# Kernel optimization log

Hardware: AMD Instinct MI355X
Metric: run time of the kernel (lower is better)

The kernel has to match this reference:

```python
import jax, jax.numpy as jnp
import numpy as np

K = 8        # number of nearest neighbors (idw default)
POWER = 2    # inverse-distance power (idw default)
EPS = 1e-8


def setup_inputs() -> dict:
    key = jax.random.key(0)
    kq, kr, kf = jax.random.split(key, 3)
    N, M = 32768, 16384
    # scale coords so points are spread out like real LiDAR scenes
    query_points = jax.random.normal(kq, (N, 3), dtype=jnp.float32) * 10.0
    ref_points = jax.random.normal(kr, (M, 3), dtype=jnp.float32) * 10.0
    ref_flow = jax.random.normal(kf, (M, 3), dtype=jnp.float32)
    return {"query_points": query_points, "ref_points": ref_points, "ref_flow": ref_flow}


def reference(query_points, ref_points, ref_flow):
    # cdist: Euclidean distance [N, M] via (q-r)^2 = |q|^2 + |r|^2 - 2 q.r
    q2 = jnp.sum(query_points * query_points, axis=-1, keepdims=True)      # [N,1]
    r2 = jnp.sum(ref_points * ref_points, axis=-1)                          # [M]
    d2 = q2 + r2 - 2.0 * (query_points @ ref_points.T)                      # [N,M]
    dist = jnp.sqrt(jnp.maximum(d2, 0.0))
    # k smallest distances == top_k of negated distances
    neg_knn, knn_idx = jax.lax.top_k(-dist, K)                               # [N,K]
    knn_dist = -neg_knn
    # inverse-distance weights: 1 / (d^power + eps), normalized over k
    weights = 1.0 / (knn_dist ** POWER + EPS)
    weights = weights / jnp.sum(weights, axis=1, keepdims=True)
    knn_flow = ref_flow[knn_idx]                                             # [N,K,3]
    return jnp.sum(weights[..., None] * knn_flow, axis=1)                    # [N,3]
```

## Files before the change

kernel.cpp:

```cpp
#include <hip/hip_runtime.h>

#define KNN    8
#define BLOCK  256
#define TILE   2048
#define GD     32
#define NC     (GD*GD*GD)
#define EPSW   1e-8f
#define BIGF   3.4e38f

__device__ __forceinline__ void insert8(float d2, int j, float bd[KNN], int bi[KNN]) {
    if (d2 < bd[0]) {
        bd[0] = d2; bi[0] = j;
#pragma unroll
        for (int t = 0; t < KNN - 1; t++) {
            if (bd[t] < bd[t + 1]) {
                float td = bd[t]; bd[t] = bd[t + 1]; bd[t + 1] = td;
                int   ti = bi[t]; bi[t] = bi[t + 1]; bi[t + 1] = ti;
            }
        }
    }
}

__device__ __forceinline__ void ced(float& a, int& ai, float& b, int& bi) {
    if (a < b) { float t = a; a = b; b = t; int ti = ai; ai = bi; bi = ti; }
}
__device__ __forceinline__ void sort8_desc(float d[KNN], int ix[KNN]) {
    ced(d[0],ix[0],d[4],ix[4]); ced(d[1],ix[1],d[5],ix[5]);
    ced(d[2],ix[2],d[6],ix[6]); ced(d[3],ix[3],d[7],ix[7]);
    ced(d[0],ix[0],d[2],ix[2]); ced(d[1],ix[1],d[3],ix[3]);
    ced(d[4],ix[4],d[6],ix[6]); ced(d[5],ix[5],d[7],ix[7]);
    ced(d[0],ix[0],d[1],ix[1]); ced(d[2],ix[2],d[3],ix[3]);
    ced(d[4],ix[4],d[5],ix[5]); ced(d[6],ix[6],d[7],ix[7]);
}
__device__ __forceinline__ void merge_lists(float bd[KNN], int bi[KNN], int mask, bool sort_after) {
    float pd[KNN]; int pi[KNN];
#pragma unroll
    for (int j = 0; j < KNN; j++) { pd[j] = __shfl_xor(bd[j], mask); pi[j] = __shfl_xor(bi[j], mask); }
#pragma unroll
    for (int j = 0; j < KNN; j++) {
        if (pd[KNN - 1 - j] < bd[j]) { bd[j] = pd[KNN - 1 - j]; bi[j] = pi[KNN - 1 - j]; }
    }
    if (sort_after) sort8_desc(bd, bi);
}
__device__ __forceinline__ float merged_thr4(const float bd[KNN]) {
    float c[KNN], p[KNN];
#pragma unroll
    for (int j = 0; j < KNN; j++) c[j] = bd[j];
#pragma unroll
    for (int j = 0; j < KNN; j++) p[j] = __shfl_xor(c[j], 1);
#pragma unroll
    for (int j = 0; j < KNN; j++) c[j] = fminf(c[j], p[KNN - 1 - j]);
    {
        float mx, mn;
        mx = fmaxf(c[0],c[4]); mn = fminf(c[0],c[4]); c[0]=mx; c[4]=mn;
        mx = fmaxf(c[1],c[5]); mn = fminf(c[1],c[5]); c[1]=mx; c[5]=mn;
        mx = fmaxf(c[2],c[6]); mn = fminf(c[2],c[6]); c[2]=mx; c[6]=mn;
        mx = fmaxf(c[3],c[7]); mn = fminf(c[3],c[7]); c[3]=mx; c[7]=mn;
        mx = fmaxf(c[0],c[2]); mn = fminf(c[0],c[2]); c[0]=mx; c[2]=mn;
        mx = fmaxf(c[1],c[3]); mn = fminf(c[1],c[3]); c[1]=mx; c[3]=mn;
        mx = fmaxf(c[4],c[6]); mn = fminf(c[4],c[6]); c[4]=mx; c[6]=mn;
        mx = fmaxf(c[5],c[7]); mn = fminf(c[5],c[7]); c[5]=mx; c[7]=mn;
        mx = fmaxf(c[0],c[1]); mn = fminf(c[0],c[1]); c[0]=mx; c[1]=mn;
        mx = fmaxf(c[2],c[3]); mn = fminf(c[2],c[3]); c[2]=mx; c[3]=mn;
        mx = fmaxf(c[4],c[5]); mn = fminf(c[4],c[5]); c[4]=mx; c[5]=mn;
        mx = fmaxf(c[6],c[7]); mn = fminf(c[6],c[7]); c[6]=mx; c[7]=mn;
    }
#pragma unroll
    for (int j = 0; j < KNN; j++) p[j] = __shfl_xor(c[j], 2);
#pragma unroll
    for (int j = 0; j < KNN; j++) c[j] = fminf(c[j], p[KNN - 1 - j]);
    float m = c[0];
#pragma unroll
    for (int j = 1; j < KNN; j++) m = fmaxf(m, c[j]);
    return m;
}

__device__ __forceinline__ unsigned fenc(float f) {
    unsigned u = __float_as_uint(f);
    return (u & 0x80000000u) ? ~u : (u | 0x80000000u);
}
__device__ __forceinline__ float fdec(unsigned e) {
    unsigned u = (e & 0x80000000u) ? (e ^ 0x80000000u) : ~e;
    return __uint_as_float(u);
}

__device__ __forceinline__ void load_bb(const unsigned* __restrict__ bbw,
                                        float mn[3], float inv[3], float& hmin) {
    hmin = BIGF;
#pragma unroll
    for (int a = 0; a < 3; a++) {
        float lo = fdec(bbw[a]), hi = -fdec(bbw[3 + a]);
        float w = fmaxf(hi - lo, 1e-9f);
        mn[a] = lo;
        inv[a] = (float)GD / w;
        hmin = fminf(hmin, w / (float)GD);
    }
}

__device__ __forceinline__ int cell_clamp(int c) {
    return c < 0 ? 0 : (c > GD - 1 ? GD - 1 : c);
}


__global__ __launch_bounds__(256) void bbox_zero(const float* __restrict__ r, int M,
                                                 unsigned* __restrict__ bbw,
                                                 int* __restrict__ zbase, int zcount) {
    int idx = blockIdx.x * 256 + threadIdx.x;
    for (int j = idx; j < zcount; j += gridDim.x * 256) zbase[j] = 0;
    float mn0 = BIGF, mn1 = BIGF, mn2 = BIGF;
    float mx0 = -BIGF, mx1 = -BIGF, mx2 = -BIGF;
    for (int j = idx; j < M; j += gridDim.x * 256) {
        float x = r[3 * j], y = r[3 * j + 1], z = r[3 * j + 2];
        mn0 = fminf(mn0, x); mx0 = fmaxf(mx0, x);
        mn1 = fminf(mn1, y); mx1 = fmaxf(mx1, y);
        mn2 = fminf(mn2, z); mx2 = fmaxf(mx2, z);
    }
#pragma unroll
    for (int o = 32; o > 0; o >>= 1) {
        mn0 = fminf(mn0, __shfl_xor(mn0, o));
        mn1 = fminf(mn1, __shfl_xor(mn1, o));
        mn2 = fminf(mn2, __shfl_xor(mn2, o));
        mx0 = fmaxf(mx0, __shfl_xor(mx0, o));
        mx1 = fmaxf(mx1, __shfl_xor(mx1, o));
        mx2 = fmaxf(mx2, __shfl_xor(mx2, o));
    }
    if ((threadIdx.x & 63) == 0) {
        atomicMin(bbw + 0, fenc(mn0)); atomicMin(bbw + 1, fenc(mn1)); atomicMin(bbw + 2, fenc(mn2));
        atomicMin(bbw + 3, fenc(-mx0)); atomicMin(bbw + 4, fenc(-mx1)); atomicMin(bbw + 5, fenc(-mx2));
    }
}

__global__ __launch_bounds__(256) void hist2(const float* __restrict__ r,
                                             const float* __restrict__ q,
                                             int M, int N, const unsigned* __restrict__ bbw,
                                             int* __restrict__ rcid, int* __restrict__ qcid,
                                             int* __restrict__ rcnt, int* __restrict__ qcnt) {
    float mn[3], inv[3], hmin;
    load_bb(bbw, mn, inv, hmin);
    int i = blockIdx.x * 256 + threadIdx.x;
    if (i < M) {
        int cx = cell_clamp((int)((r[3 * i]     - mn[0]) * inv[0]));
        int cy = cell_clamp((int)((r[3 * i + 1] - mn[1]) * inv[1]));
        int cz = cell_clamp((int)((r[3 * i + 2] - mn[2]) * inv[2]));
        int cid = (cz * GD + cy) * GD + cx;
        rcid[i] = cid;
        atomicAdd(rcnt + cid, 1);
    } else if (i < M + N) {
        int j = i - M;
        int cx = cell_clamp((int)((q[3 * j]     - mn[0]) * inv[0]));
        int cy = cell_clamp((int)((q[3 * j + 1] - mn[1]) * inv[1]));
        int cz = cell_clamp((int)((q[3 * j + 2] - mn[2]) * inv[2]));
        int cid = (cz * GD + cy) * GD + cx;
        qcid[j] = cid;
        atomicAdd(qcnt + cid, 1);
    }
}

__global__ __launch_bounds__(1024) void scan2(int* __restrict__ rcnt, int* __restrict__ rstart,
                                              int* __restrict__ qcnt, int* __restrict__ qstart) {
    int* cnt = (blockIdx.x == 0) ? rcnt : qcnt;
    int* st  = (blockIdx.x == 0) ? rstart : qstart;
    __shared__ int part[1024];
    int t = threadIdx.x;
    int base = t * 32;
    int s = 0;
#pragma unroll
    for (int k = 0; k < 32; k++) s += cnt[base + k];
    part[t] = s;
    __syncthreads();
    for (int off = 1; off < 1024; off <<= 1) {
        int v = (t >= off) ? part[t - off] : 0;
        __syncthreads();
        part[t] += v;
        __syncthreads();
    }
    int run = part[t] - s;
#pragma unroll
    for (int k = 0; k < 32; k++) {
        int c = cnt[base + k];
        st[base + k] = run;
        cnt[base + k] = run;
        run += c;
    }
    if (t == 1023) st[NC] = run;
}

__global__ __launch_bounds__(256) void scatter2(const float* __restrict__ r,
                                                const float* __restrict__ q, int M, int N,
                                                const int* __restrict__ rcid,
                                                const int* __restrict__ qcid,
                                                int* __restrict__ rcur, int* __restrict__ qcur,
                                                float4* __restrict__ rps, int* __restrict__ sidx,
                                                float4* __restrict__ qps, int* __restrict__ qorder) {
    int i = blockIdx.x * 256 + threadIdx.x;
    if (i < M) {
        int pos = atomicAdd(rcur + rcid[i], 1);
        float x = r[3 * i], y = r[3 * i + 1], z = r[3 * i + 2];
        rps[pos] = make_float4(x, y, z, x * x + y * y + z * z);
        sidx[pos] = i;
    } else if (i < M + N) {
        int j = i - M;
        int pos = atomicAdd(qcur + qcid[j], 1);
        float x = q[3 * j], y = q[3 * j + 1], z = q[3 * j + 2];
        qps[pos] = make_float4(x, y, z, x * x + y * y + z * z);
        qorder[pos] = j;
    }
}

__device__ __forceinline__ void scan_shell(
    int R, int cx, int cy, int cz, int sub,
    const float4* __restrict__ rps, const int* __restrict__ rstart,
    float qx, float qy, float qz, float q2,
    float bd[KNN], int bi[KNN], float& thr) {
    for (int dz = -R; dz <= R; ++dz) {
        int z = cz + dz;
        if ((unsigned)z >= GD) continue;
        for (int dy = -R; dy <= R; ++dy) {
            int y = cy + dy;
            if ((unsigned)y >= GD) continue;
            int rowb = (z * GD + y) * GD;
            if (dz == -R || dz == R || dy == -R || dy == R) {
                int x0 = max(cx - R, 0), x1 = min(cx + R, GD - 1);
                int s = rstart[rowb + x0], e = rstart[rowb + x1 + 1];
                for (int ii = s + sub; ii < e; ii += 4) {
                    float4 p = rps[ii];
                    float d2 = (q2 + p.w) - 2.0f * (qx * p.x + qy * p.y + qz * p.z);
                    if (d2 < thr) { insert8(d2, ii, bd, bi); thr = bd[0]; }
                }
            } else {
                int xl = cx - R, xr = cx + R;
                if (xl >= 0) {
                    int s = rstart[rowb + xl], e = rstart[rowb + xl + 1];
                    for (int ii = s + sub; ii < e; ii += 4) {
                        float4 p = rps[ii];
                        float d2 = (q2 + p.w) - 2.0f * (qx * p.x + qy * p.y + qz * p.z);
                        if (d2 < thr) { insert8(d2, ii, bd, bi); thr = bd[0]; }
                    }
                }
                if (xr < GD) {
                    int s = rstart[rowb + xr], e = rstart[rowb + xr + 1];
                    for (int ii = s + sub; ii < e; ii += 4) {
                        float4 p = rps[ii];
                        float d2 = (q2 + p.w) - 2.0f * (qx * p.x + qy * p.y + qz * p.z);
                        if (d2 < thr) { insert8(d2, ii, bd, bi); thr = bd[0]; }
                    }
                }
            }
        }
    }
}

__global__ __launch_bounds__(256) void knn_pass1(
    const float4* __restrict__ rps, const int* __restrict__ rstart,
    const float4* __restrict__ qps, const int* __restrict__ qorder,
    const int* __restrict__ sidx, const float* __restrict__ f,
    const unsigned* __restrict__ bbw, float* __restrict__ out,
    int* __restrict__ pend, int* __restrict__ pcnt, int N) {
    int t = blockIdx.x * 256 + threadIdx.x;
    int g = t >> 2;
    int sub = t & 3;
    if (g >= N) return;
    int qi = qorder[g];
    float4 qp = qps[g];
    float qx = qp.x, qy = qp.y, qz = qp.z, q2 = qp.w;
    float mn[3], inv[3], hmin;
    load_bb(bbw, mn, inv, hmin);
    int cx = cell_clamp((int)((qx - mn[0]) * inv[0]));
    int cy = cell_clamp((int)((qy - mn[1]) * inv[1]));
    int cz = cell_clamp((int)((qz - mn[2]) * inv[2]));

    float bd[KNN]; int bi[KNN];
#pragma unroll
    for (int k = 0; k < KNN; k++) { bd[k] = BIGF; bi[k] = 0; }
    float thr = BIGF;

    int rs[9], re[9];
#pragma unroll
    for (int dz = -1; dz <= 1; dz++) {
#pragma unroll
        for (int dy = -1; dy <= 1; dy++) {
            int k = (dz + 1) * 3 + (dy + 1);
            int z = cz + dz, y = cy + dy;
            if ((unsigned)z >= GD || (unsigned)y >= GD) { rs[k] = 0; re[k] = 0; }
            else {
                int rowb = (z * GD + y) * GD;
                int x0 = max(cx - 1, 0), x1 = min(cx + 1, GD - 1);
                rs[k] = rstart[rowb + x0]; re[k] = rstart[rowb + x1 + 1];
            }
        }
    }
#pragma unroll
    for (int k = 0; k < 9; k++) {
        for (int ii = rs[k] + sub; ii < re[k]; ii += 4) {
            float4 p = rps[ii];
            float d2 = (q2 + p.w) - 2.0f * (qx * p.x + qy * p.y + qz * p.z);
            if (d2 < thr) { insert8(d2, ii, bd, bi); thr = bd[0]; }
        }
    }
    float mthr = merged_thr4(bd);
    thr = fminf(thr, mthr);
    bool done = (mthr <= hmin * hmin);

    if (!done) {
        scan_shell(2, cx, cy, cz, sub, rps, rstart, qx, qy, qz, q2, bd, bi, thr);
        mthr = merged_thr4(bd);
        done = (mthr <= 4.0f * hmin * hmin);
    }

    if (!done) {
        if (sub == 0) { int pos = atomicAdd(pcnt, 1); pend[pos] = qi; }
        return;
    }

    merge_lists(bd, bi, 1, true);
    merge_lists(bd, bi, 2, false);
    if (sub == 0) {
        float wsum = 0.f, ox = 0.f, oy = 0.f, oz = 0.f;
#pragma unroll
        for (int k = 0; k < KNN; k++) {
            float w = 1.0f / (fmaxf(bd[k], 0.0f) + EPSW);
            int j = sidx[bi[k]];
            wsum += w;
            ox += w * f[3 * j];
            oy += w * f[3 * j + 1];
            oz += w * f[3 * j + 2];
        }
        float invw = 1.0f / wsum;
        out[3 * qi]     = ox * invw;
        out[3 * qi + 1] = oy * invw;
        out[3 * qi + 2] = oz * invw;
    }
}

__global__ __launch_bounds__(256) void knn_pass2(
    const float4* __restrict__ rps, const int* __restrict__ pend,
    const int* __restrict__ pcnt, const float* __restrict__ q,
    const int* __restrict__ sidx, const float* __restrict__ f,
    float* __restrict__ out, int M) {
    __shared__ float sd[4][KNN];
    __shared__ int   si[4][KNN];
    int tid = threadIdx.x;
    int lane = tid & 63, wv = tid >> 6;
    int cnt = *pcnt;
    for (int w = blockIdx.x; w < cnt; w += gridDim.x) {
        int qi = pend[w];
        float qx = q[3 * qi], qy = q[3 * qi + 1], qz = q[3 * qi + 2];
        float q2 = qx * qx + qy * qy + qz * qz;
        float bd[KNN]; int bi[KNN];
#pragma unroll
        for (int k = 0; k < KNN; k++) { bd[k] = BIGF; bi[k] = 0; }
        float thr = BIGF;
        int i = tid;
        for (; i + 1792 < M; i += 2048) {
            float4 p0 = rps[i];
            float4 p1 = rps[i + 256];
            float4 p2 = rps[i + 512];
            float4 p3 = rps[i + 768];
            float4 p4 = rps[i + 1024];
            float4 p5 = rps[i + 1280];
            float4 p6 = rps[i + 1536];
            float4 p7 = rps[i + 1792];
            float d0 = (q2 + p0.w) - 2.0f * (qx * p0.x + qy * p0.y + qz * p0.z);
            float d1 = (q2 + p1.w) - 2.0f * (qx * p1.x + qy * p1.y + qz * p1.z);
            float d2 = (q2 + p2.w) - 2.0f * (qx * p2.x + qy * p2.y + qz * p2.z);
            float d3 = (q2 + p3.w) - 2.0f * (qx * p3.x + qy * p3.y + qz * p3.z);
            float d4 = (q2 + p4.w) - 2.0f * (qx * p4.x + qy * p4.y + qz * p4.z);
            float d5 = (q2 + p5.w) - 2.0f * (qx * p5.x + qy * p5.y + qz * p5.z);
            float d6 = (q2 + p6.w) - 2.0f * (qx * p6.x + qy * p6.y + qz * p6.z);
            float d7 = (q2 + p7.w) - 2.0f * (qx * p7.x + qy * p7.y + qz * p7.z);
            if (d0 < thr) { insert8(d0, i,        bd, bi); thr = bd[0]; }
            if (d1 < thr) { insert8(d1, i + 256,  bd, bi); thr = bd[0]; }
            if (d2 < thr) { insert8(d2, i + 512,  bd, bi); thr = bd[0]; }
            if (d3 < thr) { insert8(d3, i + 768,  bd, bi); thr = bd[0]; }
            if (d4 < thr) { insert8(d4, i + 1024, bd, bi); thr = bd[0]; }
            if (d5 < thr) { insert8(d5, i + 1280, bd, bi); thr = bd[0]; }
            if (d6 < thr) { insert8(d6, i + 1536, bd, bi); thr = bd[0]; }
            if (d7 < thr) { insert8(d7, i + 1792, bd, bi); thr = bd[0]; }
        }
        for (; i < M; i += 256) {
            float4 p = rps[i];
            float d2 = (q2 + p.w) - 2.0f * (qx * p.x + qy * p.y + qz * p.z);
            if (d2 < thr) { insert8(d2, i, bd, bi); thr = bd[0]; }
        }
        merge_lists(bd, bi, 1, true);
        merge_lists(bd, bi, 2, true);
        merge_lists(bd, bi, 4, true);
        merge_lists(bd, bi, 8, true);
        merge_lists(bd, bi, 16, true);
        merge_lists(bd, bi, 32, true);
        if (lane == 0) {
#pragma unroll
            for (int k = 0; k < KNN; k++) { sd[wv][k] = bd[k]; si[wv][k] = bi[k]; }
        }
        __syncthreads();
        if (tid == 0) {
            for (int v = 1; v < 4; v++) {
#pragma unroll
                for (int k = 0; k < KNN; k++) insert8(sd[v][k], si[v][k], bd, bi);
            }
            float wsum = 0.f, ox = 0.f, oy = 0.f, oz = 0.f;
#pragma unroll
            for (int k = 0; k < KNN; k++) {
                float wgt = 1.0f / (fmaxf(bd[k], 0.0f) + EPSW);
                int j = sidx[bi[k]];
                wsum += wgt;
                ox += wgt * f[3 * j];
                oy += wgt * f[3 * j + 1];
                oz += wgt * f[3 * j + 2];
            }
            float invw = 1.0f / wsum;
            out[3 * qi]     = ox * invw;
            out[3 * qi + 1] = oy * invw;
            out[3 * qi + 2] = oz * invw;
        }
        __syncthreads();
    }
}

__global__ __launch_bounds__(BLOCK) void knn_fused(
    const float* __restrict__ q, const float* __restrict__ r,
    const float* __restrict__ f, float* __restrict__ out, int N, int M) {
    __shared__ float4 lds[TILE];
    int qi = blockIdx.x * BLOCK + threadIdx.x;
    float qx = 0.f, qy = 0.f, qz = 0.f, q2 = 0.f;
    if (qi < N) {
        qx = q[3 * qi]; qy = q[3 * qi + 1]; qz = q[3 * qi + 2];
        q2 = qx * qx + qy * qy + qz * qz;
    }
    float bd[KNN]; int bi[KNN];
#pragma unroll
    for (int k = 0; k < KNN; k++) { bd[k] = BIGF; bi[k] = 0; }
    for (int tb = 0; tb < M; tb += TILE) {
        int cnt = min(TILE, M - tb);
        for (int i = threadIdx.x; i < cnt; i += BLOCK) {
            int j = tb + i;
            float rx = r[3 * j], ry = r[3 * j + 1], rz = r[3 * j + 2];
            lds[i] = make_float4(rx, ry, rz, rx * rx + ry * ry + rz * rz);
        }
        __syncthreads();
        for (int i = 0; i < cnt; i++) {
            float4 p = lds[i];
            float d2 = (q2 + p.w) - 2.0f * (qx * p.x + qy * p.y + qz * p.z);
            insert8(d2, tb + i, bd, bi);
        }
        __syncthreads();
    }
    if (qi < N) {
        float wsum = 0.f, ox = 0.f, oy = 0.f, oz = 0.f;
#pragma unroll
        for (int k = 0; k < KNN; k++) {
            float w = 1.0f / (fmaxf(bd[k], 0.0f) + EPSW);
            int j = bi[k];
            ox += w * f[3 * j];
            oy += w * f[3 * j + 1];
            oz += w * f[3 * j + 2];
        }
        float inv = 1.0f / wsum;
        out[3 * qi]     = ox * inv;
        out[3 * qi + 1] = oy * inv;
        out[3 * qi + 2] = oz * inv;
    }
}

extern "C" void kernel_launch(void* const* d_in, const int* in_sizes, int n_in,
                              void* d_out, int out_size, void* d_ws, size_t ws_size,
                              hipStream_t stream) {
    const float* q = (const float*)d_in[0];
    const float* r = (const float*)d_in[1];
    const float* f = (const float*)d_in[2];
    float* out = (float*)d_out;
    int N = in_sizes[0] / 3;
    int M = in_sizes[1] / 3;

    size_t off = 0;
    auto take = [&](size_t b) { size_t o = off; off += (b + 255) & ~(size_t)255; return o; };
    size_t o_rps  = take((size_t)M * 16);
    size_t o_qps  = take((size_t)N * 16);
    size_t o_sidx = take((size_t)M * 4);
    size_t o_rcid = take((size_t)M * 4);
    size_t o_qcid = take((size_t)N * 4);
    size_t o_qord = take((size_t)N * 4);
    size_t o_rst  = take((size_t)(NC + 1) * 4);
    size_t o_qst  = take((size_t)(NC + 1) * 4);
    size_t o_rcur = take((size_t)NC * 4);
    size_t o_qcur = take((size_t)NC * 4);
    size_t o_pcnt = take(4);
    size_t o_pend = take((size_t)N * 4);
    size_t o_bb   = take(64);

    int grid_x = (N + BLOCK - 1) / BLOCK;
    if (off <= ws_size) {
        char* w = (char*)d_ws;
        float4* rps   = (float4*)(w + o_rps);
        float4* qps   = (float4*)(w + o_qps);
        int* sidx     = (int*)(w + o_sidx);
        int* rcid     = (int*)(w + o_rcid);
        int* qcid     = (int*)(w + o_qcid);
        int* qorder   = (int*)(w + o_qord);
        int* rstart   = (int*)(w + o_rst);
        int* qstart   = (int*)(w + o_qst);
        int* rcur     = (int*)(w + o_rcur);
        int* qcur     = (int*)(w + o_qcur);
        int* pcnt     = (int*)(w + o_pcnt);
        int* pend     = (int*)(w + o_pend);
        unsigned* bbw = (unsigned*)(w + o_bb);

        hipMemsetAsync(w + o_bb, 0xFF, 24, stream);

        int zcount = (int)((o_pcnt + 4 - o_rcur) / 4);
        int g_all = (M + N + 255) / 256;
        bbox_zero<<<64, 256, 0, stream>>>(r, M, bbw, rcur, zcount);
        hist2<<<g_all, 256, 0, stream>>>(r, q, M, N, bbw, rcid, qcid, rcur, qcur);
        scan2<<<2, 1024, 0, stream>>>(rcur, rstart, qcur, qstart);
        scatter2<<<g_all, 256, 0, stream>>>(r, q, M, N, rcid, qcid, rcur, qcur,
                                            rps, sidx, qps, qorder);
        int g_p1 = (int)(((size_t)N * 4 + 255) / 256);
        knn_pass1<<<g_p1, 256, 0, stream>>>(rps, rstart, qps, qorder, sidx, f, bbw, out,
                                            pend, pcnt, N);
        knn_pass2<<<4096, 256, 0, stream>>>(rps, pend, pcnt, q, sidx, f, out, M);
    } else {
        knn_fused<<<grid_x, BLOCK, 0, stream>>>(q, r, f, out, N, M);
    }
}
```

Measured before the change: 196.8 us.

## Fuse grid-build kernels into one cooperative kernel with grid syncs

Replaces the memset plus bbox, histogram, scan and scatter launches with a single cooperative kernel of 256 blocks that separates the phases with grid-wide syncs. The aim is to remove per-launch overhead and inter-kernel gaps in the preprocessing stage. In exchange, the scan runs with 256 threads per block, each handling more cells serially. Grid syncs add their own cost, and the cooperative launch needs all 256 blocks to be co-resident on the device.

```diff
diff --git a/kernel.cpp b/kernel.cpp
--- a/kernel.cpp
+++ b/kernel.cpp
@@ -1,4 +1,7 @@
 #include <hip/hip_runtime.h>
+#include <hip/hip_cooperative_groups.h>
+
+namespace cg = cooperative_groups;
 
 #define KNN    8
 #define BLOCK  256
@@ -101,109 +104,114 @@
     return c < 0 ? 0 : (c > GD - 1 ? GD - 1 : c);
 }
 
-
-__global__ __launch_bounds__(256) void bbox_zero(const float* __restrict__ r, int M,
-                                                 unsigned* __restrict__ bbw,
-                                                 int* __restrict__ zbase, int zcount) {
+__global__ __launch_bounds__(256) void grid_build(
+    const float* __restrict__ r, const float* __restrict__ q, int M, int N,
+    unsigned* __restrict__ bbw,
+    int* __restrict__ rcid, int* __restrict__ qcid,
+    int* __restrict__ rcnt, int* __restrict__ qcnt,
+    int* __restrict__ rstart, int* __restrict__ qstart,
+    float4* __restrict__ rps, int* __restrict__ sidx,
+    float4* __restrict__ qps, int* __restrict__ qorder,
+    int* __restrict__ pcnt) {
+    cg::grid_group grid = cg::this_grid();
+    __shared__ int part[256];
     int idx = blockIdx.x * 256 + threadIdx.x;
-    for (int j = idx; j < zcount; j += gridDim.x * 256) zbase[j] = 0;
-    float mn0 = BIGF, mn1 = BIGF, mn2 = BIGF;
-    float mx0 = -BIGF, mx1 = -BIGF, mx2 = -BIGF;
-    for (int j = idx; j < M; j += gridDim.x * 256) {
-        float x = r[3 * j], y = r[3 * j + 1], z = r[3 * j + 2];
-        mn0 = fminf(mn0, x); mx0 = fmaxf(mx0, x);
-        mn1 = fminf(mn1, y); mx1 = fmaxf(mx1, y);
-        mn2 = fminf(mn2, z); mx2 = fmaxf(mx2, z);
-    }
-#pragma unroll
-    for (int o = 32; o > 0; o >>= 1) {
-        mn0 = fminf(mn0, __shfl_xor(mn0, o));
-        mn1 = fminf(mn1, __shfl_xor(mn1, o));
-        mn2 = fminf(mn2, __shfl_xor(mn2, o));
-        mx0 = fmaxf(mx0, __shfl_xor(mx0, o));
-        mx1 = fmaxf(mx1, __shfl_xor(mx1, o));
-        mx2 = fmaxf(mx2, __shfl_xor(mx2, o));
-    }
-    if ((threadIdx.x & 63) == 0) {
-        atomicMin(bbw + 0, fenc(mn0)); atomicMin(bbw + 1, fenc(mn1)); atomicMin(bbw + 2, fenc(mn2));
-        atomicMin(bbw + 3, fenc(-mx0)); atomicMin(bbw + 4, fenc(-mx1)); atomicMin(bbw + 5, fenc(-mx2));
-    }
-}
-
-__global__ __launch_bounds__(256) void hist2(const float* __restrict__ r,
-                                             const float* __restrict__ q,
-                                             int M, int N, const unsigned* __restrict__ bbw,
-                                             int* __restrict__ rcid, int* __restrict__ qcid,
-                                             int* __restrict__ rcnt, int* __restrict__ qcnt) {
-    float mn[3], inv[3], hmin;
-    load_bb(bbw, mn, inv, hmin);
-    int i = blockIdx.x * 256 + threadIdx.x;
-    if (i < M) {
-        int cx = cell_clamp((int)((r[3 * i]     - mn[0]) * inv[0]));
-        int cy = cell_clamp((int)((r[3 * i + 1] - mn[1]) * inv[1]));
-        int cz = cell_clamp((int)((r[3 * i + 2] - mn[2]) * inv[2]));
-        int cid = (cz * GD + cy) * GD + cx;
-        rcid[i] = cid;
-        atomicAdd(rcnt + cid, 1);
-    } else if (i < M + N) {
-        int j = i - M;
-        int cx = cell_clamp((int)((q[3 * j]     - mn[0]) * inv[0]));
-        int cy = cell_clamp((int)((q[3 * j + 1] - mn[1]) * inv[1]));
-        int cz = cell_clamp((int)((q[3 * j + 2] - mn[2]) * inv[2]));
-        int cid = (cz * GD + cy) * GD + cx;
-        qcid[j] = cid;
-        atomicAdd(qcnt + cid, 1);
-    }
-}
-
-__global__ __launch_bounds__(1024) void scan2(int* __restrict__ rcnt, int* __restrict__ rstart,
-                                              int* __restrict__ qcnt, int* __restrict__ qstart) {
-    int* cnt = (blockIdx.x == 0) ? rcnt : qcnt;
-    int* st  = (blockIdx.x == 0) ? rstart : qstart;
-    __shared__ int part[1024];
-    int t = threadIdx.x;
-    int base = t * 32;
-    int s = 0;
-#pragma unroll
-    for (int k = 0; k < 32; k++) s += cnt[base + k];
-    part[t] = s;
-    __syncthreads();
-    for (int off = 1; off < 1024; off <<= 1) {
-        int v = (t >= off) ? part[t - off] : 0;
+    int nthr = gridDim.x * 256;
+
+    for (int i = idx; i < NC; i += nthr) { rcnt[i] = 0; qcnt[i] = 0; }
+    if (idx == 0) *pcnt = 0;
+    if (idx < 6) bbw[idx] = 0xFFFFFFFFu;
+    grid.sync();
+
+    {
+        float mn0 = BIGF, mn1 = BIGF, mn2 = BIGF;
+        float mx0 = -BIGF, mx1 = -BIGF, mx2 = -BIGF;
+        for (int j = idx; j < M; j += nthr) {
+            float x = r[3 * j], y = r[3 * j + 1], z = r[3 * j + 2];
+            mn0 = fminf(mn0, x); mx0 = fmaxf(mx0, x);
+            mn1 = fminf(mn1, y); mx1 = fmaxf(mx1, y);
+            mn2 = fminf(mn2, z); mx2 = fmaxf(mx2, z);
+        }
+#pragma unroll
+        for (int o = 32; o > 0; o >>= 1) {
+            mn0 = fminf(mn0, __shfl_xor(mn0, o));
+            mn1 = fminf(mn1, __shfl_xor(mn1, o));
+            mn2 = fminf(mn2, __shfl_xor(mn2, o));
+            mx0 = fmaxf(mx0, __shfl_xor(mx0, o));
+            mx1 = fmaxf(mx1, __shfl_xor(mx1, o));
+            mx2 = fmaxf(mx2, __shfl_xor(mx2, o));
+        }
+        if ((threadIdx.x & 63) == 0) {
+            atomicMin(bbw + 0, fenc(mn0)); atomicMin(bbw + 1, fenc(mn1)); atomicMin(bbw + 2, fenc(mn2));
+            atomicMin(bbw + 3, fenc(-mx0)); atomicMin(bbw + 4, fenc(-mx1)); atomicMin(bbw + 5, fenc(-mx2));
+        }
+    }
+    grid.sync();
+
+    {
+        float mn[3], inv[3], hmin;
+        load_bb(bbw, mn, inv, hmin);
+        for (int i = idx; i < M + N; i += nthr) {
+            if (i < M) {
+                int cx = cell_clamp((int)((r[3 * i]     - mn[0]) * inv[0]));
+                int cy = cell_clamp((int)((r[3 * i + 1] - mn[1]) * inv[1]));
+                int cz = cell_clamp((int)((r[3 * i + 2] - mn[2]) * inv[2]));
+                int cid = (cz * GD + cy) * GD + cx;
+                rcid[i] = cid;
+                atomicAdd(rcnt + cid, 1);
+            } else {
+                int j = i - M;
+                int cx = cell_clamp((int)((q[3 * j]     - mn[0]) * inv[0]));
+                int cy = cell_clamp((int)((q[3 * j + 1] - mn[1]) * inv[1]));
+                int cz = cell_clamp((int)((q[3 * j + 2] - mn[2]) * inv[2]));
+                int cid = (cz * GD + cy) * GD + cx;
+                qcid[j] = cid;
+                atomicAdd(qcnt + cid, 1);
+            }
+        }
+    }
+    grid.sync();
+
+    if (blockIdx.x < 2) {
+        int* cnt = (blockIdx.x == 0) ? rcnt : qcnt;
+        int* st  = (blockIdx.x == 0) ? rstart : qstart;
+        int t = threadIdx.x;
+        const int CPT = NC / 256;
+        int base = t * CPT;
+        int s = 0;
+        for (int k = 0; k < CPT; k++) s += cnt[base + k];
+        part[t] = s;
         __syncthreads();
-        part[t] += v;
-        __syncthreads();
-    }
-    int run = part[t] - s;
-#pragma unroll
-    for (int k = 0; k < 32; k++) {
-        int c = cnt[base + k];
-        st[base + k] = run;
-        cnt[base + k] = run;
-        run += c;
-    }
-    if (t == 1023) st[NC] = run;
-}
-
-__global__ __launch_bounds__(256) void scatter2(const float* __restrict__ r,
-                                                const float* __restrict__ q, int M, int N,
-                                                const int* __restrict__ rcid,
-                                                const int* __restrict__ qcid,
-                                                int* __restrict__ rcur, int* __restrict__ qcur,
-                                                float4* __restrict__ rps, int* __restrict__ sidx,
-                                                float4* __restrict__ qps, int* __restrict__ qorder) {
-    int i = blockIdx.x * 256 + threadIdx.x;
-    if (i < M) {
-        int pos = atomicAdd(rcur + rcid[i], 1);
-        float x = r[3 * i], y = r[3 * i + 1], z = r[3 * i + 2];
-        rps[pos] = make_float4(x, y, z, x * x + y * y + z * z);
-        sidx[pos] = i;
-    } else if (i < M + N) {
-        int j = i - M;
-        int pos = atomicAdd(qcur + qcid[j], 1);
-        float x = q[3 * j], y = q[3 * j + 1], z = q[3 * j + 2];
-        qps[pos] = make_float4(x, y, z, x * x + y * y + z * z);
-        qorder[pos] = j;
+        for (int off = 1; off < 256; off <<= 1) {
+            int v = (t >= off) ? part[t - off] : 0;
+            __syncthreads();
+            part[t] += v;
+            __syncthreads();
+        }
+        int run = part[t] - s;
+        for (int k = 0; k < CPT; k++) {
+            int c = cnt[base + k];
+            st[base + k] = run;
+            cnt[base + k] = run;
+            run += c;
+        }
+        if (t == 255) st[NC] = run;
+    }
+    grid.sync();
+
+    for (int i = idx; i < M + N; i += nthr) {
+        if (i < M) {
+            int pos = atomicAdd(rcnt + rcid[i], 1);
+            float x = r[3 * i], y = r[3 * i + 1], z = r[3 * i + 2];
+            rps[pos] = make_float4(x, y, z, x * x + y * y + z * z);
+            sidx[pos] = i;
+        } else {
+            int j = i - M;
+            int pos = atomicAdd(qcnt + qcid[j], 1);
+            float x = q[3 * j], y = q[3 * j + 1], z = q[3 * j + 2];
+            qps[pos] = make_float4(x, y, z, x * x + y * y + z * z);
+            qorder[pos] = j;
+        }
     }
 }
 
@@ -505,15 +513,13 @@
         int* pend     = (int*)(w + o_pend);
         unsigned* bbw = (unsigned*)(w + o_bb);
 
-        hipMemsetAsync(w + o_bb, 0xFF, 24, stream);
-
-        int zcount = (int)((o_pcnt + 4 - o_rcur) / 4);
-        int g_all = (M + N + 255) / 256;
-        bbox_zero<<<64, 256, 0, stream>>>(r, M, bbw, rcur, zcount);
-        hist2<<<g_all, 256, 0, stream>>>(r, q, M, N, bbw, rcid, qcid, rcur, qcur);
-        scan2<<<2, 1024, 0, stream>>>(rcur, rstart, qcur, qstart);
-        scatter2<<<g_all, 256, 0, stream>>>(r, q, M, N, rcid, qcid, rcur, qcur,
-                                            rps, sidx, qps, qorder);
+        void* args[] = {(void*)&r, (void*)&q, (void*)&M, (void*)&N, (void*)&bbw,
+                        (void*)&rcid, (void*)&qcid, (void*)&rcur, (void*)&qcur,
+                        (void*)&rstart, (void*)&qstart, (void*)&rps, (void*)&sidx,
+                        (void*)&qps, (void*)&qorder, (void*)&pcnt};
+        hipLaunchCooperativeKernel((void*)grid_build, dim3(256), dim3(256),
+                                   args, 0, stream);
+
         int g_p1 = (int)(((size_t)N * 4 + 255) / 256);
         knn_pass1<<<g_p1, 256, 0, stream>>>(rps, rstart, qps, qorder, sidx, f, bbw, out,
                                             pend, pcnt, N);
```

Measured after the change: 342.3 us. +74.0%, slower.
